# Performance work log

Measured on AMD Instinct MI355X. Metric: run time of the kernel, lower is better.

## Reference

```python
import jax, jax.numpy as jnp
import numpy as np

_D, _R = 1024, 4096


def flow_multinomial(n, p):
    """n: [...], p: [..., k] -> mean [..., k], cov [..., k, k]."""
    mean = n[..., None] * p  # [..., k]
    k = p.shape[-1]
    eye = jnp.eye(k, dtype=p.dtype)
    # diag(mean) - n * p p^T
    cov = mean[..., None] * eye - n[..., None, None] * (p[..., :, None] * p[..., None, :])
    return mean, cov


def mvn_logprob(x, mean, cov):
    """Batched MVN log-prob via Cholesky. x/mean: [..., k], cov: [..., k, k]."""
    k = x.shape[-1]
    L = jnp.linalg.cholesky(cov)
    diff = (x - mean)[..., None]  # [..., k, 1]
    z = jax.lax.linalg.triangular_solve(L, diff, left_side=True, lower=True)
    quad = jnp.sum(z[..., 0] ** 2, axis=-1)
    logdet = 2.0 * jnp.sum(jnp.log(jnp.diagonal(L, axis1=-2, axis2=-1)), axis=-1)
    return -0.5 * (k * jnp.log(2.0 * jnp.pi) + logdet + quad)


def setup_inputs() -> dict:
    D, R = _D, _R
    key = jax.random.key(0)
    ks = jax.random.split(key, 20)
    u = lambda k, shape, lo, hi: jax.random.uniform(k, shape, minval=lo, maxval=hi, dtype=jnp.float32)
    N = u(ks[0], (R,), 1e6, 2e6)
    S = N * u(ks[1], (D, R), 0.4, 0.7)
    E = N * u(ks[2], (D, R), 0.005, 0.02)
    I = N * u(ks[3], (D, R), 0.005, 0.02)
    T = N * u(ks[4], (D, R), 0.002, 0.01)
    # observed flows for each transition (any finite values are valid)
    S_E = S[:-1] * u(ks[5], (D - 1, R), 0.0, 0.02)
    E_I = E[:-1] * u(ks[6], (D - 1, R), 0.1, 0.4)
    I_T = I[:-1] * u(ks[7], (D - 1, R), 0.1, 0.3)
    I_U = I[:-1] * u(ks[8], (D - 1, R), 0.1, 0.3)
    T_R = T[:-1] * u(ks[9], (D - 1, R), 0.2, 0.5)
    T_D = T[:-1] * u(ks[10], (D - 1, R), 0.0, 0.05)
    adjacency = u(ks[11], (R, R), 0.0, 1.0)
    logit_decay_E = jax.random.normal(ks[12], (), dtype=jnp.float32)
    logit_decay_I = jax.random.normal(ks[13], (), dtype=jnp.float32)
    logit_decay_T = jax.random.normal(ks[14], (), dtype=jnp.float32)
    detection_rate = u(ks[15], (D, R), 0.05, 0.95)
    recovery_rate = u(ks[16], (D, R), 0.05, 0.95)
    contagion_I = u(ks[17], (D, R), 0.1, 2.0)
    return dict(S=S, E=E, I=I, T=T, N=N, S_E=S_E, E_I=E_I, I_T=I_T, I_U=I_U,
                T_R=T_R, T_D=T_D, adjacency=adjacency,
                logit_decay_E=logit_decay_E, logit_decay_I=logit_decay_I,
                logit_decay_T=logit_decay_T, detection_rate=detection_rate,
                recovery_rate=recovery_rate, contagion_I=contagion_I)


def reference(S, E, I, T, N, S_E, E_I, I_T, I_U, T_R, T_D, adjacency,
              logit_decay_E, logit_decay_I, logit_decay_T,
              detection_rate, recovery_rate, contagion_I):
    decay_E = jax.nn.sigmoid(logit_decay_E)
    decay_I = jax.nn.sigmoid(logit_decay_I)
    decay_T = jax.nn.sigmoid(logit_decay_T)

    # states at the start of each transition t = 0 .. D-2
    So, Eo, Io, To = S[:-1], E[:-1], I[:-1], T[:-1]  # [D-1, R]

    # prob_S_E, vectorized over transitions: A @ I_t for each t
    AI = jnp.einsum('rq,tq->tr', adjacency, Io)       # [D-1, R]
    AN = adjacency @ N                                 # [R]
    p_SE = -jnp.expm1(-(contagion_I[:-1] * AI) / AN)   # [D-1, R]

    # S -> E (1-dim MVN)
    mS, cS = flow_multinomial(So, p_SE[..., None])
    lpS = mvn_logprob(S_E[..., None], mS, cS)

    # E -> I (1-dim MVN)
    p_EI = jnp.broadcast_to(decay_E, p_SE.shape)
    mE, cE = flow_multinomial(Eo, p_EI[..., None])
    lpE = mvn_logprob(E_I[..., None], mE, cE)

    # I -> (T, U) (2-dim MVN)
    det = detection_rate[:-1]
    pI = jnp.stack([det * decay_I, (1.0 - det) * decay_I], axis=-1)  # [D-1, R, 2]
    mI, cI = flow_multinomial(Io, pI)
    lpI = mvn_logprob(jnp.stack([I_T, I_U], axis=-1), mI, cI)

    # T -> (R, D) (2-dim MVN)
    rec = recovery_rate[:-1]
    pT = jnp.stack([rec * decay_T, (1.0 - rec) * decay_T], axis=-1)
    mT, cT = flow_multinomial(To, pT)
    lpT = mvn_logprob(jnp.stack([T_R, T_D], axis=-1), mT, cT)

    # sum over transitions -> per-region total log prob [R]
    return jnp.sum(lpS + lpE + lpI + lpT, axis=0)
```

## Files before the change

### kernel.cpp

```cpp
#include <hip/hip_runtime.h>
#include <hip/hip_bf16.h>
#include <math.h>

typedef __attribute__((ext_vector_type(8))) short bf16x8;
typedef __attribute__((ext_vector_type(4))) float f32x4;
typedef unsigned int u32;

__device__ inline ushort f2bf(float x) {
  union { float f; unsigned u; } c; c.f = x;
  unsigned u = c.u;
  u += 0x7fffu + ((u >> 16) & 1u);
  return (ushort)(u >> 16);
}

__device__ __forceinline__ float rcpf(float x) { return __builtin_amdgcn_rcpf(x); }

__device__ __forceinline__ void gl_lds16(const ushort* g, ushort* l) {
  __builtin_amdgcn_global_load_lds(
      (const __attribute__((address_space(1))) u32*)g,
      (__attribute__((address_space(3))) u32*)l, 16, 0, 0);
}

__global__ __launch_bounds__(256) void conv_fused(const float* __restrict__ adj,
                                                  const float* __restrict__ Nv,
                                                  const float* __restrict__ I,
                                                  ushort* __restrict__ adjbf,
                                                  ushort* __restrict__ Ibf,
                                                  float* __restrict__ AN,
                                                  int R, int nI) {
  const int bx = blockIdx.x;
  const int tid = threadIdx.x;
  if (bx < R) {
    const int r = bx;
    const float* row = adj + (size_t)r * R;
    ushort* orow = adjbf + (size_t)r * R;
    float acc = 0.f;
    for (int q0 = tid * 4; q0 < R; q0 += 256 * 4) {
      float4 v = *(const float4*)(row + q0);
      float4 nv = *(const float4*)(Nv + q0);
      acc += v.x * nv.x + v.y * nv.y + v.z * nv.z + v.w * nv.w;
      ushort4 o;
      o.x = f2bf(v.x); o.y = f2bf(v.y); o.z = f2bf(v.z); o.w = f2bf(v.w);
      *(ushort4*)(orow + q0) = o;
    }
    #pragma unroll
    for (int off = 32; off > 0; off >>= 1) acc += __shfl_down(acc, off, 64);
    __shared__ float red[4];
    if ((tid & 63) == 0) red[tid >> 6] = acc;
    __syncthreads();
    if (tid == 0) AN[r] = red[0] + red[1] + red[2] + red[3];
  } else {
    int i = ((bx - R) * 256 + tid) * 4;
    if (i + 3 < nI) {
      float4 v = *(const float4*)(I + i);
      ushort4 o;
      o.x = f2bf(v.x); o.y = f2bf(v.y); o.z = f2bf(v.z); o.w = f2bf(v.w);
      *(ushort4*)(Ibf + i) = o;
    }
  }
}

__global__ __launch_bounds__(256) void gemm_bt_lds(const ushort* __restrict__ A,
                                                   const ushort* __restrict__ B,
                                                   float* __restrict__ C,
                                                   int M, int N, int K, int Ksplit) {
  __shared__ __align__(16) ushort sA[2][128 * 32];
  __shared__ __align__(16) ushort sB[2][128 * 32];
  const int tid = threadIdx.x;
  const int bn = blockIdx.x, bm = blockIdx.y, bz = blockIdx.z;
  const int wave = tid >> 6, lane = tid & 63;
  const int wm = (wave >> 1) * 64, wn = (wave & 1) * 64;

  const int p0 = wave * 2, p1 = wave * 2 + 1;
  const int lrow = lane >> 2;
  const int sblk = (lane & 3) ^ (lrow & 3);
  const int scol = sblk * 8;
  const size_t kbase = (size_t)bz * Ksplit + scol;
  const ushort* Ag0 = A + (size_t)(bm * 128 + p0 * 16 + lrow) * K + kbase;
  const ushort* Ag1 = A + (size_t)(bm * 128 + p1 * 16 + lrow) * K + kbase;
  const ushort* Bg0 = B + (size_t)(bn * 128 + p0 * 16 + lrow) * K + kbase;
  const ushort* Bg1 = B + (size_t)(bn * 128 + p1 * 16 + lrow) * K + kbase;
  const int lo0 = p0 * 16 * 32;
  const int lo1 = p1 * 16 * 32;

  const int fm = lane & 15;
  const int fkb = lane >> 4;
  const int pblk = (fkb ^ (fm & 3)) * 8;

  f32x4 acc[4][4];
  #pragma unroll
  for (int i = 0; i < 4; ++i)
    #pragma unroll
    for (int j = 0; j < 4; ++j) acc[i][j] = (f32x4){0.f, 0.f, 0.f, 0.f};

  auto STAGE = [&](int b, int k0) {
    gl_lds16(Ag0 + k0, sA[b] + lo0);
    gl_lds16(Ag1 + k0, sA[b] + lo1);
    gl_lds16(Bg0 + k0, sB[b] + lo0);
    gl_lds16(Bg1 + k0, sB[b] + lo1);
  };
  auto COMPUTE = [&](int b) {
    bf16x8 af[4], bfr[4];
    #pragma unroll
    for (int i = 0; i < 4; ++i)
      af[i] = *(const bf16x8*)(sA[b] + (wm + i * 16 + fm) * 32 + pblk);
    #pragma unroll
    for (int j = 0; j < 4; ++j)
      bfr[j] = *(const bf16x8*)(sB[b] + (wn + j * 16 + fm) * 32 + pblk);
    #pragma unroll
    for (int i = 0; i < 4; ++i)
      #pragma unroll
      for (int j = 0; j < 4; ++j)
        acc[i][j] = __builtin_amdgcn_mfma_f32_16x16x32_bf16(af[i], bfr[j], acc[i][j], 0, 0, 0);
  };

  STAGE(0, 0);
  __syncthreads();
  int cur = 0;
  for (int k0 = 0; k0 + 32 < Ksplit; k0 += 32) {
    STAGE(cur ^ 1, k0 + 32);
    COMPUTE(cur);
    __syncthreads();
    cur ^= 1;
  }
  COMPUTE(cur);

  float* Cz = C + (size_t)bz * M * N;
  const int cm = (lane >> 4) * 4, cn = lane & 15;
  #pragma unroll
  for (int i = 0; i < 4; ++i)
    #pragma unroll
    for (int j = 0; j < 4; ++j) {
      size_t base = (size_t)(bm * 128 + wm + i * 16 + cm) * N + (bn * 128 + wn + j * 16 + cn);
      #pragma unroll
      for (int v = 0; v < 4; ++v)
        Cz[base + (size_t)v * N] = acc[i][j][v];
    }
}

__device__ __forceinline__ float elem_ll(float Sv, float Ev, float Iv, float Tv,
                                         float sev, float eiv, float itv, float iuv,
                                         float trv, float tdv, float dev, float rev,
                                         float cov, float aiv, float ran_,
                                         float dE, float omE, float dI, float omI,
                                         float dT, float omT) {
  float p = -expm1f(-(cov * aiv) * ran_);
  float mS = Sv * p;
  float varS = mS * (1.f - p);
  float dS = sev - mS;
  float mE = Ev * dE;
  float varE = mE * omE;
  float dEd = eiv - mE;
  float p1 = dev * dI, p2 = (1.f - dev) * dI;
  float d1 = itv - Iv * p1;
  float d2 = iuv - Iv * p2;
  float denI = Iv * p1 * p2 * omI;
  float qI = (d1 * d1 * p2 * (1.f - p2) + 2.f * d1 * d2 * p1 * p2 +
              d2 * d2 * p1 * (1.f - p1)) * rcpf(denI);
  float q1 = rev * dT, q2 = (1.f - rev) * dT;
  float e1 = trv - Tv * q1;
  float e2 = tdv - Tv * q2;
  float denT = Tv * q1 * q2 * omT;
  float qT = (e1 * e1 * q2 * (1.f - q2) + 2.f * e1 * e2 * q1 * q2 +
              e2 * e2 * q1 * (1.f - q1)) * rcpf(denT);

  float quad = dS * dS * rcpf(varS) + dEd * dEd * rcpf(varE) + qI + qT;
  float lg = __logf((varS * varE) * ((Iv * denI) * (Tv * denT)));
  return lg + quad;
}

template <int NS>
__global__ __launch_bounds__(256, 4) void logprob_kernel(
    const float* __restrict__ S, const float* __restrict__ E,
    const float* __restrict__ I, const float* __restrict__ T,
    const float* __restrict__ S_E, const float* __restrict__ E_I,
    const float* __restrict__ I_T, const float* __restrict__ I_U,
    const float* __restrict__ T_R, const float* __restrict__ T_D,
    const float* __restrict__ detr, const float* __restrict__ recr,
    const float* __restrict__ cont, const float* __restrict__ AI,
    const float* __restrict__ AN,
    const float* __restrict__ pldE, const float* __restrict__ pldI,
    const float* __restrict__ pldT, float* __restrict__ partial, int D1, int R) {
  const int r0 = (blockIdx.x * 256 + threadIdx.x) * 4;
  const size_t sstride = (size_t)(D1 + 1) * R;
  const float dE = 1.f / (1.f + __expf(-pldE[0]));
  const float dI = 1.f / (1.f + __expf(-pldI[0]));
  const float dT = 1.f / (1.f + __expf(-pldT[0]));
  const float omE = 1.f - dE, omI = 1.f - dI, omT = 1.f - dT;
  const float L2PI = 1.8378770664093453f;
  float4 an4 = *(const float4*)(AN + r0);
  float ran_[4] = {rcpf(an4.x), rcpf(an4.y), rcpf(an4.z), rcpf(an4.w)};

  const int t0 = blockIdx.y * 2;
  const bool two = (t0 + 1 < D1);
  const float wB = two ? 1.f : 0.f;
  const size_t iA = (size_t)t0 * R + r0;
  const size_t iB = iA + (two ? (size_t)R : 0);

#define LD4(arr, i) (*(const float4*)((arr) + (i)))
  float4 SvA = LD4(S, iA),   SvB = LD4(S, iB);
  float4 EvA = LD4(E, iA),   EvB = LD4(E, iB);
  float4 IvA = LD4(I, iA),   IvB = LD4(I, iB);
  float4 TvA = LD4(T, iA),   TvB = LD4(T, iB);
  float4 seA = LD4(S_E, iA), seB = LD4(S_E, iB);
  float4 eiA = LD4(E_I, iA), eiB = LD4(E_I, iB);
  float4 itA = LD4(I_T, iA), itB = LD4(I_T, iB);
  float4 iuA = LD4(I_U, iA), iuB = LD4(I_U, iB);
  float4 trA = LD4(T_R, iA), trB = LD4(T_R, iB);
  float4 tdA = LD4(T_D, iA), tdB = LD4(T_D, iB);
  float4 deA = LD4(detr, iA), deB = LD4(detr, iB);
  float4 reA = LD4(recr, iA), reB = LD4(recr, iB);
  float4 coA = LD4(cont, iA), coB = LD4(cont, iB);

  float aiA[4] = {0.f, 0.f, 0.f, 0.f};
  float aiB[4] = {0.f, 0.f, 0.f, 0.f};
  #pragma unroll
  for (int s = 0; s < NS; ++s) {
    float4 a = LD4(AI, s * sstride + iA);
    float4 b = LD4(AI, s * sstride + iB);
    aiA[0] += a.x; aiA[1] += a.y; aiA[2] += a.z; aiA[3] += a.w;
    aiB[0] += b.x; aiB[1] += b.y; aiB[2] += b.z; aiB[3] += b.w;
  }
#undef LD4

  float accA[4], accB[4];
  {
    float Sa[4] = {SvA.x, SvA.y, SvA.z, SvA.w}, Ea[4] = {EvA.x, EvA.y, EvA.z, EvA.w};
    float Ia[4] = {IvA.x, IvA.y, IvA.z, IvA.w}, Ta[4] = {TvA.x, TvA.y, TvA.z, TvA.w};
    float sea[4] = {seA.x, seA.y, seA.z, seA.w}, eia[4] = {eiA.x, eiA.y, eiA.z, eiA.w};
    float ita[4] = {itA.x, itA.y, itA.z, itA.w}, iua[4] = {iuA.x, iuA.y, iuA.z, iuA.w};
    float tra[4] = {trA.x, trA.y, trA.z, trA.w}, tda[4] = {tdA.x, tdA.y, tdA.z, tdA.w};
    float dea[4] = {deA.x, deA.y, deA.z, deA.w}, rea[4] = {reA.x, reA.y, reA.z, reA.w};
    float coa[4] = {coA.x, coA.y, coA.z, coA.w};
    #pragma unroll
    for (int v = 0; v < 4; ++v)
      accA[v] = elem_ll(Sa[v], Ea[v], Ia[v], Ta[v], sea[v], eia[v], ita[v], iua[v],
                        tra[v], tda[v], dea[v], rea[v], coa[v], aiA[v], ran_[v],
                        dE, omE, dI, omI, dT, omT);
  }
  {
    float Sa[4] = {SvB.x, SvB.y, SvB.z, SvB.w}, Ea[4] = {EvB.x, EvB.y, EvB.z, EvB.w};
    float Ia[4] = {IvB.x, IvB.y, IvB.z, IvB.w}, Ta[4] = {TvB.x, TvB.y, TvB.z, TvB.w};
    float sea[4] = {seB.x, seB.y, seB.z, seB.w}, eia[4] = {eiB.x, eiB.y, eiB.z, eiB.w};
    float ita[4] = {itB.x, itB.y, itB.z, itB.w}, iua[4] = {iuB.x, iuB.y, iuB.z, iuB.w};
    float tra[4] = {trB.x, trB.y, trB.z, trB.w}, tda[4] = {tdB.x, tdB.y, tdB.z, tdB.w};
    float dea[4] = {deB.x, deB.y, deB.z, deB.w}, rea[4] = {reB.x, reB.y, reB.z, reB.w};
    float coa[4] = {coB.x, coB.y, coB.z, coB.w};
    #pragma unroll
    for (int v = 0; v < 4; ++v)
      accB[v] = elem_ll(Sa[v], Ea[v], Ia[v], Ta[v], sea[v], eia[v], ita[v], iua[v],
                        tra[v], tda[v], dea[v], rea[v], coa[v], aiB[v], ran_[v],
                        dE, omE, dI, omI, dT, omT);
  }

  const float cterm = -3.f * L2PI * (two ? 2.f : 1.f);
  float4 res;
  res.x = -0.5f * (accA[0] + wB * accB[0]) + cterm;
  res.y = -0.5f * (accA[1] + wB * accB[1]) + cterm;
  res.z = -0.5f * (accA[2] + wB * accB[2]) + cterm;
  res.w = -0.5f * (accA[3] + wB * accB[3]) + cterm;
  *(float4*)(partial + (size_t)blockIdx.y * R + r0) = res;
}

__global__ __launch_bounds__(256) void reduce_kernel(const float* __restrict__ part,
                                                     float* __restrict__ out,
                                                     int R, int NBY) {
  __shared__ float red[256];
  const int tid = threadIdx.x;
  const int r = blockIdx.x * 32 + (tid & 31);
  const int slice = tid >> 5;
  const int rows = NBY >> 3;
  float acc = 0.f;
  for (int k = 0; k < rows; ++k)
    acc += part[(size_t)(slice * rows + k) * R + r];
  red[tid] = acc;
  __syncthreads();
  if (tid < 32) {
    float s = red[tid];
    #pragma unroll
    for (int sl = 1; sl < 8; ++sl) s += red[sl * 32 + tid];
    out[r] = s;
  }
}

extern "C" void kernel_launch(void* const* d_in, const int* in_sizes, int n_in,
                              void* d_out, int out_size, void* d_ws, size_t ws_size,
                              hipStream_t stream) {
  const float* S    = (const float*)d_in[0];
  const float* E    = (const float*)d_in[1];
  const float* I    = (const float*)d_in[2];
  const float* T    = (const float*)d_in[3];
  const float* Nv   = (const float*)d_in[4];
  const float* S_E  = (const float*)d_in[5];
  const float* E_I  = (const float*)d_in[6];
  const float* I_T  = (const float*)d_in[7];
  const float* I_U  = (const float*)d_in[8];
  const float* T_R  = (const float*)d_in[9];
  const float* T_D  = (const float*)d_in[10];
  const float* adj  = (const float*)d_in[11];
  const float* ldE  = (const float*)d_in[12];
  const float* ldI  = (const float*)d_in[13];
  const float* ldT  = (const float*)d_in[14];
  const float* detr = (const float*)d_in[15];
  const float* recr = (const float*)d_in[16];
  const float* cont = (const float*)d_in[17];
  float* out = (float*)d_out;

  const int R  = in_sizes[4];
  const int D  = in_sizes[0] / R;
  const int D1 = D - 1;
  const int NBY = (D1 + 1) / 2;

  char* ws = (char*)d_ws;
  ushort* adjbf = (ushort*)ws;
  ushort* Ibf   = (ushort*)(ws + (size_t)R * R * 2);
  float*  AIbuf = (float*)(ws + (size_t)R * R * 2 + (size_t)D * R * 2);
  const size_t tail = (size_t)R * 4 + (size_t)NBY * R * 4;
  const size_t need4 = (size_t)R * R * 2 + (size_t)D * R * 2 +
                       4 * (size_t)D * R * 4 + tail;
  const int NS = (ws_size >= need4) ? 4 : 2;
  float* ANbuf   = (float*)((char*)AIbuf + (size_t)NS * D * R * 4);
  float* partial = ANbuf + R;

  const int nI = D * R;
  const int convBlocks = R + nI / (256 * 4);
  hipLaunchKernelGGL(conv_fused, dim3(convBlocks), dim3(256), 0, stream,
                     adj, Nv, I, adjbf, Ibf, ANbuf, R, nI);
  hipLaunchKernelGGL(gemm_bt_lds, dim3(R / 128, D / 128, NS), dim3(256), 0, stream,
                     Ibf, adjbf, AIbuf, D, R, R, R / NS);
  if (NS == 4) {
    hipLaunchKernelGGL(logprob_kernel<4>, dim3(R / 1024, NBY), dim3(256), 0, stream,
                       S, E, I, T, S_E, E_I, I_T, I_U, T_R, T_D, detr, recr, cont,
                       AIbuf, ANbuf, ldE, ldI, ldT, partial, D1, R);
  } else {
    hipLaunchKernelGGL(logprob_kernel<2>, dim3(R / 1024, NBY), dim3(256), 0, stream,
                       S, E, I, T, S_E, E_I, I_T, I_U, T_R, T_D, detr, recr, cont,
                       AIbuf, ANbuf, ldE, ldI, ldT, partial, D1, R);
  }
  hipLaunchKernelGGL(reduce_kernel, dim3(R / 32), dim3(256), 0, stream,
                     partial, out, R, NBY);
}
```

Measured before the change: 355.3 us.

## Replace partial-sum buffer and reduce kernel with atomic accumulation into output

The per-region sum over transition pairs no longer goes through a partial buffer and a separate reduce kernel. Each logprob block now atomically adds its four results straight into the output, which the conversion kernel zeroes first. The GEMM split-K is also fixed at 2 rather than chosen as 4 when workspace allows, giving fewer split partial AI buffers to write and read. This saves a kernel launch and a partial-buffer round trip, at the cost of 512-way atomic contention per output element and a summation order that is no longer deterministic.

```diff
diff --git a/kernel.cpp b/kernel.cpp
--- a/kernel.cpp
+++ b/kernel.cpp
@@ -27,6 +27,7 @@
                                                   ushort* __restrict__ adjbf,
                                                   ushort* __restrict__ Ibf,
                                                   float* __restrict__ AN,
+                                                  float* __restrict__ out,
                                                   int R, int nI) {
   const int bx = blockIdx.x;
   const int tid = threadIdx.x;
@@ -50,6 +51,10 @@
     __syncthreads();
     if (tid == 0) AN[r] = red[0] + red[1] + red[2] + red[3];
   } else {
+    if (bx == R) {
+      float4 z = {0.f, 0.f, 0.f, 0.f};
+      for (int k = tid; k < R / 4; k += 256) ((float4*)out)[k] = z;
+    }
     int i = ((bx - R) * 256 + tid) * 4;
     if (i + 3 < nI) {
       float4 v = *(const float4*)(I + i);
@@ -180,7 +185,7 @@
     const float* __restrict__ cont, const float* __restrict__ AI,
     const float* __restrict__ AN,
     const float* __restrict__ pldE, const float* __restrict__ pldI,
-    const float* __restrict__ pldT, float* __restrict__ partial, int D1, int R) {
+    const float* __restrict__ pldT, float* __restrict__ out, int D1, int R) {
   const int r0 = (blockIdx.x * 256 + threadIdx.x) * 4;
   const size_t sstride = (size_t)(D1 + 1) * R;
   const float dE = 1.f / (1.f + __expf(-pldE[0]));
@@ -254,33 +259,10 @@
   }
 
   const float cterm = -3.f * L2PI * (two ? 2.f : 1.f);
-  float4 res;
-  res.x = -0.5f * (accA[0] + wB * accB[0]) + cterm;
-  res.y = -0.5f * (accA[1] + wB * accB[1]) + cterm;
-  res.z = -0.5f * (accA[2] + wB * accB[2]) + cterm;
-  res.w = -0.5f * (accA[3] + wB * accB[3]) + cterm;
-  *(float4*)(partial + (size_t)blockIdx.y * R + r0) = res;
-}
-
-__global__ __launch_bounds__(256) void reduce_kernel(const float* __restrict__ part,
-                                                     float* __restrict__ out,
-                                                     int R, int NBY) {
-  __shared__ float red[256];
-  const int tid = threadIdx.x;
-  const int r = blockIdx.x * 32 + (tid & 31);
-  const int slice = tid >> 5;
-  const int rows = NBY >> 3;
-  float acc = 0.f;
-  for (int k = 0; k < rows; ++k)
-    acc += part[(size_t)(slice * rows + k) * R + r];
-  red[tid] = acc;
-  __syncthreads();
-  if (tid < 32) {
-    float s = red[tid];
-    #pragma unroll
-    for (int sl = 1; sl < 8; ++sl) s += red[sl * 32 + tid];
-    out[r] = s;
-  }
+  atomicAdd(&out[r0 + 0], -0.5f * (accA[0] + wB * accB[0]) + cterm);
+  atomicAdd(&out[r0 + 1], -0.5f * (accA[1] + wB * accB[1]) + cterm);
+  atomicAdd(&out[r0 + 2], -0.5f * (accA[2] + wB * accB[2]) + cterm);
+  atomicAdd(&out[r0 + 3], -0.5f * (accA[3] + wB * accB[3]) + cterm);
 }
 
 extern "C" void kernel_launch(void* const* d_in, const int* in_sizes, int n_in,
@@ -310,33 +292,21 @@
   const int D  = in_sizes[0] / R;
   const int D1 = D - 1;
   const int NBY = (D1 + 1) / 2;
+  const int NS = 2;
 
   char* ws = (char*)d_ws;
   ushort* adjbf = (ushort*)ws;
   ushort* Ibf   = (ushort*)(ws + (size_t)R * R * 2);
   float*  AIbuf = (float*)(ws + (size_t)R * R * 2 + (size_t)D * R * 2);
-  const size_t tail = (size_t)R * 4 + (size_t)NBY * R * 4;
-  const size_t need4 = (size_t)R * R * 2 + (size_t)D * R * 2 +
-                       4 * (size_t)D * R * 4 + tail;
-  const int NS = (ws_size >= need4) ? 4 : 2;
-  float* ANbuf   = (float*)((char*)AIbuf + (size_t)NS * D * R * 4);
-  float* partial = ANbuf + R;
+  float*  ANbuf = (float*)((char*)AIbuf + (size_t)NS * D * R * 4);
 
   const int nI = D * R;
   const int convBlocks = R + nI / (256 * 4);
   hipLaunchKernelGGL(conv_fused, dim3(convBlocks), dim3(256), 0, stream,
-                     adj, Nv, I, adjbf, Ibf, ANbuf, R, nI);
+                     adj, Nv, I, adjbf, Ibf, ANbuf, out, R, nI);
   hipLaunchKernelGGL(gemm_bt_lds, dim3(R / 128, D / 128, NS), dim3(256), 0, stream,
                      Ibf, adjbf, AIbuf, D, R, R, R / NS);
-  if (NS == 4) {
-    hipLaunchKernelGGL(logprob_kernel<4>, dim3(R / 1024, NBY), dim3(256), 0, stream,
-                       S, E, I, T, S_E, E_I, I_T, I_U, T_R, T_D, detr, recr, cont,
-                       AIbuf, ANbuf, ldE, ldI, ldT, partial, D1, R);
-  } else {
-    hipLaunchKernelGGL(logprob_kernel<2>, dim3(R / 1024, NBY), dim3(256), 0, stream,
-                       S, E, I, T, S_E, E_I, I_T, I_U, T_R, T_D, detr, recr, cont,
-                       AIbuf, ANbuf, ldE, ldI, ldT, partial, D1, R);
-  }
-  hipLaunchKernelGGL(reduce_kernel, dim3(R / 32), dim3(256), 0, stream,
-                     partial, out, R, NBY);
-}
+  hipLaunchKernelGGL(logprob_kernel<2>, dim3(R / 1024, NBY), dim3(256), 0, stream,
+                     S, E, I, T, S_E, E_I, I_T, I_U, T_R, T_D, detr, recr, cont,
+                     AIbuf, ANbuf, ldE, ldI, ldT, out, D1, R);
+}
```

New measurement: 364.2 us. +2.5%, slower.
